# Optimization experiments

Hardware: AMD Instinct MI355X
Metric: run time of the kernel (lower is better)

## Reference

```python
import jax, jax.numpy as jnp
import numpy as np

H = 8          # num_heads
WIN = 63       # win_size
LEFT = WIN - 1 - WIN // 2  # 31
EPS = 1e-5


def layer_norm(x, w, b):
    mu = x.mean(-1, keepdims=True)
    var = ((x - mu) ** 2).mean(-1, keepdims=True)
    return (x - mu) / jnp.sqrt(var + EPS) * w + b


def setup_inputs() -> dict:
    key = jax.random.key(0)
    N, T, C = 2, 2048, 512
    hid = 4 * C
    ks = jax.random.split(key, 16)
    s = 0.02
    return {
        "x": jax.random.normal(ks[0], (N, T, C), jnp.float32),
        "norm1_w": jnp.ones((C,), jnp.float32),
        "norm1_b": jnp.zeros((C,), jnp.float32),
        "qkv_w": jax.random.normal(ks[1], (3 * C, C), jnp.float32) * s,
        "qkv_b": jnp.zeros((3 * C,), jnp.float32),
        "rel_bias": jax.random.normal(ks[2], (H, WIN), jnp.float32) * s,
        "proj_w": jax.random.normal(ks[3], (C, C), jnp.float32) * s,
        "proj_b": jnp.zeros((C,), jnp.float32),
        "norm2_w": jnp.ones((C,), jnp.float32),
        "norm2_b": jnp.zeros((C,), jnp.float32),
        "fc1_w": jax.random.normal(ks[4], (hid, C), jnp.float32) * s,
        "fc1_b": jnp.zeros((hid,), jnp.float32),
        "fc2_w": jax.random.normal(ks[5], (C, hid), jnp.float32) * s,
        "fc2_b": jnp.zeros((C,), jnp.float32),
    }


def reference(x, norm1_w, norm1_b, qkv_w, qkv_b, rel_bias, proj_w, proj_b,
              norm2_w, norm2_b, fc1_w, fc1_b, fc2_w, fc2_b):
    N, T, C = x.shape
    hd = C // H
    scale = hd ** -0.5
    right = WIN - LEFT - 1

    shortcut = x
    h = layer_norm(x, norm1_w, norm1_b)
    qkv = (h @ qkv_w.T + qkv_b).reshape(N, T, 3, H, hd)
    q, k, v = qkv[:, :, 0], qkv[:, :, 1], qkv[:, :, 2]  # (N,T,H,hd)

    # zero-pad keys/values along time, gather sliding windows
    kp = jnp.pad(k, ((0, 0), (LEFT, right), (0, 0), (0, 0)))
    vp = jnp.pad(v, ((0, 0), (LEFT, right), (0, 0), (0, 0)))
    idx = jnp.arange(T)[:, None] + jnp.arange(WIN)[None, :]
    k_win = kp[:, idx]
    v_win = vp[:, idx]

    attn = jnp.einsum('nthd,ntwhd->nhtw', q * scale, k_win)
    attn = attn + rel_bias[None, :, None, :]
    # boundary mask: key position j = t - LEFT + w must lie in [0, T)
    pos = idx - LEFT
    mask = jnp.where((pos < 0) | (pos >= T), jnp.float32(-100.0), jnp.float32(0.0))
    attn = attn + mask[None, None, :, :]
    attn = jax.nn.softmax(attn, axis=-1)

    out = jnp.einsum('nhtw,ntwhd->nthd', attn, v_win).reshape(N, T, C)
    out = out @ proj_w.T + proj_b

    x = shortcut + out
    h2 = layer_norm(x, norm2_w, norm2_b)
    m = jax.nn.gelu(h2 @ fc1_w.T + fc1_b, approximate=False)  # torch nn.GELU = exact erf
    m = m @ fc2_w.T + fc2_b
    return x + m
```

## Files before the change

kernel.cpp:

```cpp
#include <hip/hip_runtime.h>

typedef unsigned short u16;
typedef unsigned int uint;
typedef __attribute__((ext_vector_type(4))) float floatx4;
typedef __attribute__((ext_vector_type(16))) float floatx16;
typedef __attribute__((ext_vector_type(8))) short shortx8;

__device__ __forceinline__ u16 f2b(float f) {
    unsigned int u = __float_as_uint(f);
    unsigned int r = (u + 0x7fffu + ((u >> 16) & 1u)) >> 16;
    return (u16)r;
}
__device__ __forceinline__ float b2f(u16 u) {
    return __uint_as_float(((unsigned int)u) << 16);
}
__device__ __forceinline__ void gl_lds16(const u16* g, u16* l) {
    __builtin_amdgcn_global_load_lds(
        (const __attribute__((address_space(1))) void*)g,
        (__attribute__((address_space(3))) void*)l, 16, 0, 0);
}
__device__ __forceinline__ float gelu_f(float v) {
    float e = __expf(1.59576912f * v * (1.0f + 0.044715f * v * v));
    return v * e / (e + 1.0f);
}

__device__ __forceinline__ void ln_row_wave_f32(const float* __restrict__ x,
                                                const float* __restrict__ w,
                                                const float* __restrict__ b,
                                                u16* __restrict__ out, int row) {
    int lane = threadIdx.x & 63;
    const float4* xr = (const float4*)(x + (size_t)row * 512);
    float4 v0 = xr[lane * 2], v1 = xr[lane * 2 + 1];
    float s = v0.x + v0.y + v0.z + v0.w + v1.x + v1.y + v1.z + v1.w;
    float s2 = v0.x * v0.x + v0.y * v0.y + v0.z * v0.z + v0.w * v0.w +
               v1.x * v1.x + v1.y * v1.y + v1.z * v1.z + v1.w * v1.w;
    #pragma unroll
    for (int o = 32; o > 0; o >>= 1) {
        s += __shfl_xor(s, o, 64);
        s2 += __shfl_xor(s2, o, 64);
    }
    float mu = s * (1.0f / 512.0f);
    float var = s2 * (1.0f / 512.0f) - mu * mu;
    float rstd = rsqrtf(var + 1e-5f);
    const float4* wr = (const float4*)w;
    const float4* br = (const float4*)b;
    float4 w0 = wr[lane * 2], w1 = wr[lane * 2 + 1];
    float4 b0 = br[lane * 2], b1 = br[lane * 2 + 1];
    uint4 o4;
    o4.x = (uint)f2b((v0.x - mu) * rstd * w0.x + b0.x) |
           ((uint)f2b((v0.y - mu) * rstd * w0.y + b0.y) << 16);
    o4.y = (uint)f2b((v0.z - mu) * rstd * w0.z + b0.z) |
           ((uint)f2b((v0.w - mu) * rstd * w0.w + b0.w) << 16);
    o4.z = (uint)f2b((v1.x - mu) * rstd * w1.x + b1.x) |
           ((uint)f2b((v1.y - mu) * rstd * w1.y + b1.y) << 16);
    o4.w = (uint)f2b((v1.z - mu) * rstd * w1.z + b1.z) |
           ((uint)f2b((v1.w - mu) * rstd * w1.w + b1.w) << 16);
    ((uint4*)(out + (size_t)row * 512))[lane] = o4;
}

__global__ __launch_bounds__(256) void ln_kernel_b(const u16* __restrict__ x,
                                                   const float* __restrict__ w,
                                                   const float* __restrict__ b,
                                                   u16* __restrict__ out) {
    int row = blockIdx.x * 4 + (threadIdx.x >> 6);
    int lane = threadIdx.x & 63;
    uint4 p = ((const uint4*)(x + (size_t)row * 512))[lane];
    float v[8];
    v[0] = b2f((u16)(p.x & 0xffffu)); v[1] = b2f((u16)(p.x >> 16));
    v[2] = b2f((u16)(p.y & 0xffffu)); v[3] = b2f((u16)(p.y >> 16));
    v[4] = b2f((u16)(p.z & 0xffffu)); v[5] = b2f((u16)(p.z >> 16));
    v[6] = b2f((u16)(p.w & 0xffffu)); v[7] = b2f((u16)(p.w >> 16));
    float s = 0.f, s2 = 0.f;
    #pragma unroll
    for (int i = 0; i < 8; i++) { s += v[i]; s2 += v[i] * v[i]; }
    #pragma unroll
    for (int o = 32; o > 0; o >>= 1) {
        s += __shfl_xor(s, o, 64);
        s2 += __shfl_xor(s2, o, 64);
    }
    float mu = s * (1.0f / 512.0f);
    float var = s2 * (1.0f / 512.0f) - mu * mu;
    float rstd = rsqrtf(var + 1e-5f);
    const float4* wr = (const float4*)w;
    const float4* br = (const float4*)b;
    float4 w0 = wr[lane * 2], w1 = wr[lane * 2 + 1];
    float4 b0 = br[lane * 2], b1 = br[lane * 2 + 1];
    float o8[8];
    o8[0] = (v[0] - mu) * rstd * w0.x + b0.x;
    o8[1] = (v[1] - mu) * rstd * w0.y + b0.y;
    o8[2] = (v[2] - mu) * rstd * w0.z + b0.z;
    o8[3] = (v[3] - mu) * rstd * w0.w + b0.w;
    o8[4] = (v[4] - mu) * rstd * w1.x + b1.x;
    o8[5] = (v[5] - mu) * rstd * w1.y + b1.y;
    o8[6] = (v[6] - mu) * rstd * w1.z + b1.z;
    o8[7] = (v[7] - mu) * rstd * w1.w + b1.w;
    uint4 o4;
    o4.x = (uint)f2b(o8[0]) | ((uint)f2b(o8[1]) << 16);
    o4.y = (uint)f2b(o8[2]) | ((uint)f2b(o8[3]) << 16);
    o4.z = (uint)f2b(o8[4]) | ((uint)f2b(o8[5]) << 16);
    o4.w = (uint)f2b(o8[6]) | ((uint)f2b(o8[7]) << 16);
    ((uint4*)(out + (size_t)row * 512))[lane] = o4;
}

__global__ __launch_bounds__(256) void prep_kernel(
    const float* __restrict__ qkvw, u16* __restrict__ wq,
    const float* __restrict__ projw, u16* __restrict__ wp,
    const float* __restrict__ fc1w, u16* __restrict__ w1,
    const float* __restrict__ fc2w, u16* __restrict__ w2,
    const float* __restrict__ x, const float* __restrict__ n1w,
    const float* __restrict__ n1b, u16* __restrict__ hb) {
    int bi = blockIdx.x;
    if (bi < 3072) {
        const float* src;
        u16* dst;
        int i0;
        if (bi < 768)       { src = qkvw; dst = wq; i0 = bi; }
        else if (bi < 1024) { src = projw; dst = wp; i0 = bi - 768; }
        else if (bi < 2048) { src = fc1w; dst = w1; i0 = bi - 1024; }
        else                { src = fc2w; dst = w2; i0 = bi - 2048; }
        int i = i0 * 256 + threadIdx.x;
        float4 v = ((const float4*)src)[i];
        uint2 o;
        o.x = (uint)f2b(v.x) | ((uint)f2b(v.y) << 16);
        o.y = (uint)f2b(v.z) | ((uint)f2b(v.w) << 16);
        ((uint2*)dst)[i] = o;
    } else {
        int row = (bi - 3072) * 4 + (threadIdx.x >> 6);
        ln_row_wave_f32(x, n1w, n1b, hb, row);
    }
}

template <int EPI>
__global__ __launch_bounds__(256, 2) void gemm16(const u16* __restrict__ A,
                                                 const u16* __restrict__ W,
                                                 const float* __restrict__ bias,
                                                 u16* __restrict__ outB,
                                                 int M, int Nn, int K) {
    constexpr int BM = 128, BN = 128, BK = 64;
    __shared__ u16 a_s[2][BM * BK];
    __shared__ u16 b_s[2][BN * BK];

    int tid = threadIdx.x;
    int wid = tid >> 6, lane = tid & 63;
    int wm = wid >> 1, wn = wid & 1;
    int m_blk = blockIdx.x * BM;
    int n_blk = blockIdx.y * BN;
    int lr = lane & 15;
    int lkc = lane >> 4;

    floatx4 acc[4][4];
    #pragma unroll
    for (int i = 0; i < 4; i++)
        #pragma unroll
        for (int j = 0; j < 4; j++) acc[i][j] = (floatx4){0.f, 0.f, 0.f, 0.f};

    const u16* Ag = A + (size_t)m_blk * K;
    const u16* Wg = W + (size_t)n_blk * K;

    int srow = tid >> 3;
    int skc = (tid & 7) ^ (srow & 7);

    auto stage = [&](int k0, int buf) {
        #pragma unroll
        for (int p = 0; p < 4; p++)
            gl_lds16(Ag + (size_t)(p * 32 + srow) * K + k0 + skc * 8,
                     a_s[buf] + (p * 256 + tid) * 8);
        #pragma unroll
        for (int p = 0; p < 4; p++)
            gl_lds16(Wg + (size_t)(p * 32 + srow) * K + k0 + skc * 8,
                     b_s[buf] + (p * 256 + tid) * 8);
    };

    stage(0, 0);
    int nit = K >> 6;
    for (int it = 0; it < nit; it++) {
        __syncthreads();
        if (it + 1 < nit) stage((it + 1) << 6, (it + 1) & 1);
        int cb = it & 1;
        #pragma unroll
        for (int s = 0; s < 2; s++) {
            int kc = s * 4 + lkc;
            shortx8 af[4], bf[4];
            #pragma unroll
            for (int i = 0; i < 4; i++) {
                int row = wm * 64 + i * 16 + lr;
                af[i] = *(const shortx8*)(a_s[cb] + (row * 8 + (kc ^ (row & 7))) * 8);
            }
            #pragma unroll
            for (int j = 0; j < 4; j++) {
                int row = wn * 64 + j * 16 + lr;
                bf[j] = *(const shortx8*)(b_s[cb] + (row * 8 + (kc ^ (row & 7))) * 8);
            }
            #pragma unroll
            for (int i = 0; i < 4; i++)
                #pragma unroll
                for (int j = 0; j < 4; j++)
                    acc[i][j] = __builtin_amdgcn_mfma_f32_16x16x32_bf16(
                        af[i], bf[j], acc[i][j], 0, 0, 0);
        }
    }

    int col_l = lane & 15;
    int row_base = (lane >> 4) * 4;
    #pragma unroll
    for (int nj = 0; nj < 4; nj++) {
        int col = n_blk + wn * 64 + nj * 16 + col_l;
        float bv = bias[col];
        #pragma unroll
        for (int mi = 0; mi < 4; mi++) {
            #pragma unroll
            for (int r = 0; r < 4; r++) {
                int row = m_blk + wm * 64 + mi * 16 + row_base + r;
                size_t off = (size_t)row * Nn + col;
                float v = acc[mi][nj][r] + bv;
                outB[off] = f2b(EPI == 2 ? gelu_f(v) : v);
            }
        }
    }
}

template <int EPI>
__global__ __launch_bounds__(256, 2) void gemm32(const u16* __restrict__ A,
                                                 const u16* __restrict__ W,
                                                 const float* __restrict__ bias,
                                                 const float* __restrict__ residF,
                                                 const u16* __restrict__ residB,
                                                 float* __restrict__ outF,
                                                 u16* __restrict__ outB,
                                                 int M, int Nn, int K) {
    constexpr int BM = 64, BN = 64, BK = 128;
    constexpr int CPR = BK / 8, KMSK = CPR - 1;
    __shared__ u16 a_s[2][BM * BK];
    __shared__ u16 b_s[2][BN * BK];

    int tid = threadIdx.x;
    int wid = tid >> 6, lane = tid & 63;
    int wm = wid >> 1, wn = wid & 1;
    int m_blk = blockIdx.x * BM;
    int n_blk = blockIdx.y * BN;
    int lr = lane & 31;
    int lk = lane >> 5;

    floatx16 acc;
    #pragma unroll
    for (int r = 0; r < 16; r++) acc[r] = 0.f;

    const u16* Ag = A + (size_t)m_blk * K;
    const u16* Wg = W + (size_t)n_blk * K;

    int srow = tid / CPR;
    int skc = (tid & KMSK) ^ (srow & KMSK);

    auto stage = [&](int k0, int buf) {
        #pragma unroll
        for (int p = 0; p < 4; p++)
            gl_lds16(Ag + (size_t)(p * 16 + srow) * K + k0 + skc * 8,
                     a_s[buf] + (p * 256 + tid) * 8);
        #pragma unroll
        for (int p = 0; p < 4; p++)
            gl_lds16(Wg + (size_t)(p * 16 + srow) * K + k0 + skc * 8,
                     b_s[buf] + (p * 256 + tid) * 8);
    };

    stage(0, 0);
    int nit = K / BK;
    for (int it = 0; it < nit; it++) {
        __syncthreads();
        if (it + 1 < nit) stage((it + 1) * BK, (it + 1) & 1);
        int cb = it & 1;
        #pragma unroll
        for (int s = 0; s < BK / 16; s++) {
            int kc = s * 2 + lk;
            int arow = wm * 32 + lr;
            int brow = wn * 32 + lr;
            shortx8 af = *(const shortx8*)(a_s[cb] + (arow * CPR + (kc ^ (arow & KMSK))) * 8);
            shortx8 bf = *(const shortx8*)(b_s[cb] + (brow * CPR + (kc ^ (brow & KMSK))) * 8);
            acc = __builtin_amdgcn_mfma_f32_32x32x16_bf16(af, bf, acc, 0, 0, 0);
        }
    }

    int col_l = lane & 31;
    int row_q = 4 * (lane >> 5);
    int col = n_blk + wn * 32 + col_l;
    float bv = bias[col];
    #pragma unroll
    for (int r = 0; r < 16; r++) {
        int row = m_blk + wm * 32 + (r & 3) + 8 * (r >> 2) + row_q;
        size_t off = (size_t)row * Nn + col;
        float v = acc[r] + bv;
        if (EPI == 1) outB[off] = f2b(v + residF[off]);
        else          outF[off] = v + b2f(residB[off]);
    }
}

__global__ __launch_bounds__(256) void attn_kernel(const u16* __restrict__ qkv,
                                                   const float* __restrict__ rel_bias,
                                                   u16* __restrict__ out) {
    __shared__ u16 k_s[128][72];
    __shared__ u16 v_t[64][152];
    __shared__ u16 p_s[4][16][104];
    __shared__ float s_bias[64];

    int bx = blockIdx.x;
    int n = bx >> 8;
    int h = (bx >> 5) & 7;
    int t0 = (bx & 31) << 6;
    int tid = threadIdx.x, wid = tid >> 6, lane = tid & 63;
    int col = lane & 15, rq = lane >> 4;

    const u16* qrow = qkv + (size_t)(n * 2048 + t0 + wid * 16 + col) * 1536 + h * 64 + rq * 8;
    shortx8 qf0 = *(const shortx8*)qrow;
    shortx8 qf1 = *(const shortx8*)(qrow + 32);

    if (tid < 63) s_bias[tid] = rel_bias[h * 63 + tid];
    if (tid == 63) s_bias[63] = 0.f;

    const uint* qkv_u = (const uint*)qkv;
    for (int idx = tid; idx < 128 * 32; idx += 256) {
        int row = idx >> 5, j = idx & 31;
        int pos = t0 - 31 + row;
        uint kv = 0;
        if (pos >= 0 && pos < 2048)
            kv = qkv_u[(size_t)(n * 2048 + pos) * 768 + 256 + h * 32 + j];
        *(uint*)&k_s[row][j * 2] = kv;
    }
    for (int idx = tid; idx < 144 * 32; idx += 256) {
        int row = idx >> 5, j = idx & 31;
        int pos = t0 - 31 + row;
        uint vv = 0;
        if (pos >= 0 && pos < 2048)
            vv = qkv_u[(size_t)(n * 2048 + pos) * 768 + 512 + h * 32 + j];
        v_t[2 * j][row] = (u16)(vv & 0xffffu);
        v_t[2 * j + 1][row] = (u16)(vv >> 16);
    }
    __syncthreads();

    floatx4 S[5];
    #pragma unroll
    for (int nt = 0; nt < 5; nt++) S[nt] = (floatx4){0.f, 0.f, 0.f, 0.f};
    #pragma unroll
    for (int nt = 0; nt < 5; nt++) {
        const u16* kb = &k_s[wid * 16 + nt * 16 + col][rq * 8];
        shortx8 b0 = *(const shortx8*)kb;
        shortx8 b1 = *(const shortx8*)(kb + 32);
        S[nt] = __builtin_amdgcn_mfma_f32_16x16x32_bf16(qf0, b0, S[nt], 0, 0, 0);
        S[nt] = __builtin_amdgcn_mfma_f32_16x16x32_bf16(qf1, b1, S[nt], 0, 0, 0);
    }

    #pragma unroll
    for (int r = 0; r < 4; r++) {
        int t_row = rq * 4 + r;
        float sc[5];
        float mx = -1e30f;
        #pragma unroll
        for (int nt = 0; nt < 5; nt++) {
            int w = nt * 16 + col - t_row;
            int pos_abs = t0 - 31 + wid * 16 + nt * 16 + col;
            float v;
            if (w < 0 || w > 62) {
                v = -1e30f;
            } else {
                v = S[nt][r] * 0.125f + s_bias[w];
                if (pos_abs < 0 || pos_abs >= 2048) v -= 100.f;
            }
            sc[nt] = v;
            mx = fmaxf(mx, v);
        }
        #pragma unroll
        for (int o = 1; o < 16; o <<= 1) mx = fmaxf(mx, __shfl_xor(mx, o, 64));
        float l = 0.f;
        #pragma unroll
        for (int nt = 0; nt < 5; nt++) {
            sc[nt] = __expf(sc[nt] - mx);
            l += sc[nt];
        }
        #pragma unroll
        for (int o = 1; o < 16; o <<= 1) l += __shfl_xor(l, o, 64);
        float inv = 1.0f / l;
        #pragma unroll
        for (int nt = 0; nt < 5; nt++)
            p_s[wid][t_row][nt * 16 + col] = f2b(sc[nt] * inv);
        p_s[wid][t_row][80 + col] = 0;
    }
    __syncthreads();

    floatx4 O[4];
    #pragma unroll
    for (int dt = 0; dt < 4; dt++) O[dt] = (floatx4){0.f, 0.f, 0.f, 0.f};
    const u16* pr = &p_s[wid][col][rq * 8];
    shortx8 a0 = *(const shortx8*)pr;
    shortx8 a1 = *(const shortx8*)(pr + 32);
    shortx8 a2 = *(const shortx8*)(pr + 64);
    #pragma unroll
    for (int dt = 0; dt < 4; dt++) {
        const u16* vb = &v_t[dt * 16 + col][wid * 16 + rq * 8];
        shortx8 b0 = *(const shortx8*)vb;
        shortx8 b1 = *(const shortx8*)(vb + 32);
        shortx8 b2 = *(const shortx8*)(vb + 64);
        O[dt] = __builtin_amdgcn_mfma_f32_16x16x32_bf16(a0, b0, O[dt], 0, 0, 0);
        O[dt] = __builtin_amdgcn_mfma_f32_16x16x32_bf16(a1, b1, O[dt], 0, 0, 0);
        O[dt] = __builtin_amdgcn_mfma_f32_16x16x32_bf16(a2, b2, O[dt], 0, 0, 0);
    }

    #pragma unroll
    for (int dt = 0; dt < 4; dt++) {
        #pragma unroll
        for (int r = 0; r < 4; r++) {
            int t_row = rq * 4 + r;
            out[(size_t)(n * 2048 + t0 + wid * 16 + t_row) * 512 + h * 64 + dt * 16 + col] =
                f2b(O[dt][r]);
        }
    }
}

extern "C" void kernel_launch(void* const* d_in, const int* in_sizes, int n_in,
                              void* d_out, int out_size, void* d_ws, size_t ws_size,
                              hipStream_t stream) {
    const float* x     = (const float*)d_in[0];
    const float* n1w   = (const float*)d_in[1];
    const float* n1b   = (const float*)d_in[2];
    const float* qkvw  = (const float*)d_in[3];
    const float* qkvbv = (const float*)d_in[4];
    const float* relb  = (const float*)d_in[5];
    const float* projw = (const float*)d_in[6];
    const float* projb = (const float*)d_in[7];
    const float* n2w   = (const float*)d_in[8];
    const float* n2b   = (const float*)d_in[9];
    const float* fc1w  = (const float*)d_in[10];
    const float* fc1b  = (const float*)d_in[11];
    const float* fc2w  = (const float*)d_in[12];
    const float* fc2b  = (const float*)d_in[13];
    float* out = (float*)d_out;

    char* p = (char*)d_ws;
    u16* wq   = (u16*)p;  p += (size_t)786432 * 2;
    u16* wp   = (u16*)p;  p += (size_t)262144 * 2;
    u16* w1   = (u16*)p;  p += (size_t)1048576 * 2;
    u16* w2   = (u16*)p;  p += (size_t)1048576 * 2;
    u16* hb   = (u16*)p;  p += (size_t)2097152 * 2;
    u16* qkvb = (u16*)p;  p += (size_t)6291456 * 2;
    u16* attb = (u16*)p;  p += (size_t)2097152 * 2;
    u16* x2b  = (u16*)p;  p += (size_t)2097152 * 2;
    u16* mb   = (u16*)p;  p += (size_t)8388608 * 2;

    prep_kernel<<<4096, 256, 0, stream>>>(qkvw, wq, projw, wp, fc1w, w1, fc2w, w2,
                                          x, n1w, n1b, hb);
    gemm16<0><<<dim3(32, 12), 256, 0, stream>>>(hb, wq, qkvbv, qkvb, 4096, 1536, 512);
    attn_kernel<<<512, 256, 0, stream>>>(qkvb, relb, attb);
    gemm32<1><<<dim3(64, 8), 256, 0, stream>>>(attb, wp, projb, x, nullptr,
                                               nullptr, x2b, 4096, 512, 512);
    ln_kernel_b<<<1024, 256, 0, stream>>>(x2b, n2w, n2b, hb);
    gemm16<2><<<dim3(32, 16), 256, 0, stream>>>(hb, w1, fc1b, mb, 4096, 2048, 512);
    gemm32<3><<<dim3(64, 8), 256, 0, stream>>>(mb, w2, fc2b, nullptr, x2b,
                                               out, nullptr, 4096, 512, 2048);
}
```

Baseline: 167.6 us.

## Drop double buffering in GEMMs and switch small GEMM to 16x16 MFMA tiles

Both GEMM kernels drop their double-buffered LDS staging and become single-buffered, with a sync before and after each K-tile compute. The 64x64 GEMM also moves from one 32x32x16 MFMA per wave with BK=128 to four 16x16x32 MFMAs per wave with BK=64. Launch bounds rise to 3 and 4 blocks per CU. The aim is to cut LDS use and raise occupancy so that other resident blocks hide memory latency, in place of in-block prefetch. The cost is that loads and compute no longer overlap within a block, and each tile needs twice as many barriers.

```diff
diff --git a/kernel.cpp b/kernel.cpp
--- a/kernel.cpp
+++ b/kernel.cpp
@@ -3,7 +3,6 @@
 typedef unsigned short u16;
 typedef unsigned int uint;
 typedef __attribute__((ext_vector_type(4))) float floatx4;
-typedef __attribute__((ext_vector_type(16))) float floatx16;
 typedef __attribute__((ext_vector_type(8))) short shortx8;
 
 __device__ __forceinline__ u16 f2b(float f) {
@@ -131,20 +130,19 @@
 }
 
 template <int EPI>
-__global__ __launch_bounds__(256, 2) void gemm16(const u16* __restrict__ A,
+__global__ __launch_bounds__(256, 3) void gemm16(const u16* __restrict__ A,
                                                  const u16* __restrict__ W,
                                                  const float* __restrict__ bias,
                                                  u16* __restrict__ outB,
                                                  int M, int Nn, int K) {
-    constexpr int BM = 128, BN = 128, BK = 64;
-    __shared__ u16 a_s[2][BM * BK];
-    __shared__ u16 b_s[2][BN * BK];
+    __shared__ u16 a_s[128 * 64];
+    __shared__ u16 b_s[128 * 64];
 
     int tid = threadIdx.x;
     int wid = tid >> 6, lane = tid & 63;
     int wm = wid >> 1, wn = wid & 1;
-    int m_blk = blockIdx.x * BM;
-    int n_blk = blockIdx.y * BN;
+    int m_blk = blockIdx.x * 128;
+    int n_blk = blockIdx.y * 128;
     int lr = lane & 15;
     int lkc = lane >> 4;
 
@@ -160,23 +158,16 @@
     int srow = tid >> 3;
     int skc = (tid & 7) ^ (srow & 7);
 
-    auto stage = [&](int k0, int buf) {
+    for (int k0 = 0; k0 < K; k0 += 64) {
         #pragma unroll
         for (int p = 0; p < 4; p++)
             gl_lds16(Ag + (size_t)(p * 32 + srow) * K + k0 + skc * 8,
-                     a_s[buf] + (p * 256 + tid) * 8);
+                     a_s + (p * 256 + tid) * 8);
         #pragma unroll
         for (int p = 0; p < 4; p++)
             gl_lds16(Wg + (size_t)(p * 32 + srow) * K + k0 + skc * 8,
-                     b_s[buf] + (p * 256 + tid) * 8);
-    };
-
-    stage(0, 0);
-    int nit = K >> 6;
-    for (int it = 0; it < nit; it++) {
+                     b_s + (p * 256 + tid) * 8);
         __syncthreads();
-        if (it + 1 < nit) stage((it + 1) << 6, (it + 1) & 1);
-        int cb = it & 1;
         #pragma unroll
         for (int s = 0; s < 2; s++) {
             int kc = s * 4 + lkc;
@@ -184,12 +175,12 @@
             #pragma unroll
             for (int i = 0; i < 4; i++) {
                 int row = wm * 64 + i * 16 + lr;
-                af[i] = *(const shortx8*)(a_s[cb] + (row * 8 + (kc ^ (row & 7))) * 8);
+                af[i] = *(const shortx8*)(a_s + (row * 8 + (kc ^ (row & 7))) * 8);
             }
             #pragma unroll
             for (int j = 0; j < 4; j++) {
                 int row = wn * 64 + j * 16 + lr;
-                bf[j] = *(const shortx8*)(b_s[cb] + (row * 8 + (kc ^ (row & 7))) * 8);
+                bf[j] = *(const shortx8*)(b_s + (row * 8 + (kc ^ (row & 7))) * 8);
             }
             #pragma unroll
             for (int i = 0; i < 4; i++)
@@ -198,6 +189,7 @@
                     acc[i][j] = __builtin_amdgcn_mfma_f32_16x16x32_bf16(
                         af[i], bf[j], acc[i][j], 0, 0, 0);
         }
+        __syncthreads();
     }
 
     int col_l = lane & 15;
@@ -220,7 +212,7 @@
 }
 
 template <int EPI>
-__global__ __launch_bounds__(256, 2) void gemm32(const u16* __restrict__ A,
+__global__ __launch_bounds__(256, 4) void gemm64(const u16* __restrict__ A,
                                                  const u16* __restrict__ W,
                                                  const float* __restrict__ bias,
                                                  const float* __restrict__ residF,
@@ -228,68 +220,80 @@
                                                  float* __restrict__ outF,
                                                  u16* __restrict__ outB,
                                                  int M, int Nn, int K) {
-    constexpr int BM = 64, BN = 64, BK = 128;
-    constexpr int CPR = BK / 8, KMSK = CPR - 1;
-    __shared__ u16 a_s[2][BM * BK];
-    __shared__ u16 b_s[2][BN * BK];
+    __shared__ u16 a_s[64 * 64];
+    __shared__ u16 b_s[64 * 64];
 
     int tid = threadIdx.x;
     int wid = tid >> 6, lane = tid & 63;
     int wm = wid >> 1, wn = wid & 1;
-    int m_blk = blockIdx.x * BM;
-    int n_blk = blockIdx.y * BN;
-    int lr = lane & 31;
-    int lk = lane >> 5;
-
-    floatx16 acc;
-    #pragma unroll
-    for (int r = 0; r < 16; r++) acc[r] = 0.f;
+    int m_blk = blockIdx.x * 64;
+    int n_blk = blockIdx.y * 64;
+    int lr = lane & 15;
+    int lkc = lane >> 4;
+
+    floatx4 acc[2][2];
+    #pragma unroll
+    for (int i = 0; i < 2; i++)
+        #pragma unroll
+        for (int j = 0; j < 2; j++) acc[i][j] = (floatx4){0.f, 0.f, 0.f, 0.f};
 
     const u16* Ag = A + (size_t)m_blk * K;
     const u16* Wg = W + (size_t)n_blk * K;
 
-    int srow = tid / CPR;
-    int skc = (tid & KMSK) ^ (srow & KMSK);
-
-    auto stage = [&](int k0, int buf) {
-        #pragma unroll
-        for (int p = 0; p < 4; p++)
-            gl_lds16(Ag + (size_t)(p * 16 + srow) * K + k0 + skc * 8,
-                     a_s[buf] + (p * 256 + tid) * 8);
-        #pragma unroll
-        for (int p = 0; p < 4; p++)
-            gl_lds16(Wg + (size_t)(p * 16 + srow) * K + k0 + skc * 8,
-                     b_s[buf] + (p * 256 + tid) * 8);
-    };
-
-    stage(0, 0);
-    int nit = K / BK;
-    for (int it = 0; it < nit; it++) {
+    int srow = tid >> 3;
+    int skc = (tid & 7) ^ (srow & 7);
+
+    for (int k0 = 0; k0 < K; k0 += 64) {
+        #pragma unroll
+        for (int p = 0; p < 2; p++)
+            gl_lds16(Ag + (size_t)(p * 32 + srow) * K + k0 + skc * 8,
+                     a_s + (p * 256 + tid) * 8);
+        #pragma unroll
+        for (int p = 0; p < 2; p++)
+            gl_lds16(Wg + (size_t)(p * 32 + srow) * K + k0 + skc * 8,
+                     b_s + (p * 256 + tid) * 8);
         __syncthreads();
-        if (it + 1 < nit) stage((it + 1) * BK, (it + 1) & 1);
-        int cb = it & 1;
-        #pragma unroll
-        for (int s = 0; s < BK / 16; s++) {
-            int kc = s * 2 + lk;
-            int arow = wm * 32 + lr;
-            int brow = wn * 32 + lr;
-            shortx8 af = *(const shortx8*)(a_s[cb] + (arow * CPR + (kc ^ (arow & KMSK))) * 8);
-            shortx8 bf = *(const shortx8*)(b_s[cb] + (brow * CPR + (kc ^ (brow & KMSK))) * 8);
-            acc = __builtin_amdgcn_mfma_f32_32x32x16_bf16(af, bf, acc, 0, 0, 0);
-        }
-    }
-
-    int col_l = lane & 31;
-    int row_q = 4 * (lane >> 5);
-    int col = n_blk + wn * 32 + col_l;
-    float bv = bias[col];
-    #pragma unroll
-    for (int r = 0; r < 16; r++) {
-        int row = m_blk + wm * 32 + (r & 3) + 8 * (r >> 2) + row_q;
-        size_t off = (size_t)row * Nn + col;
-        float v = acc[r] + bv;
-        if (EPI == 1) outB[off] = f2b(v + residF[off]);
-        else          outF[off] = v + b2f(residB[off]);
+        #pragma unroll
+        for (int s = 0; s < 2; s++) {
+            int kc = s * 4 + lkc;
+            shortx8 af[2], bf[2];
+            #pragma unroll
+            for (int i = 0; i < 2; i++) {
+                int row = wm * 32 + i * 16 + lr;
+                af[i] = *(const shortx8*)(a_s + (row * 8 + (kc ^ (row & 7))) * 8);
+            }
+            #pragma unroll
+            for (int j = 0; j < 2; j++) {
+                int row = wn * 32 + j * 16 + lr;
+                bf[j] = *(const shortx8*)(b_s + (row * 8 + (kc ^ (row & 7))) * 8);
+            }
+            #pragma unroll
+            for (int i = 0; i < 2; i++)
+                #pragma unroll
+                for (int j = 0; j < 2; j++)
+                    acc[i][j] = __builtin_amdgcn_mfma_f32_16x16x32_bf16(
+                        af[i], bf[j], acc[i][j], 0, 0, 0);
+        }
+        __syncthreads();
+    }
+
+    int col_l = lane & 15;
+    int row_base = (lane >> 4) * 4;
+    #pragma unroll
+    for (int nj = 0; nj < 2; nj++) {
+        int col = n_blk + wn * 32 + nj * 16 + col_l;
+        float bv = bias[col];
+        #pragma unroll
+        for (int mi = 0; mi < 2; mi++) {
+            #pragma unroll
+            for (int r = 0; r < 4; r++) {
+                int row = m_blk + wm * 32 + mi * 16 + row_base + r;
+                size_t off = (size_t)row * Nn + col;
+                float v = acc[mi][nj][r] + bv;
+                if (EPI == 1) outB[off] = f2b(v + residF[off]);
+                else          outF[off] = v + b2f(residB[off]);
+            }
+        }
     }
 }
 
@@ -447,10 +451,10 @@
                                           x, n1w, n1b, hb);
     gemm16<0><<<dim3(32, 12), 256, 0, stream>>>(hb, wq, qkvbv, qkvb, 4096, 1536, 512);
     attn_kernel<<<512, 256, 0, stream>>>(qkvb, relb, attb);
-    gemm32<1><<<dim3(64, 8), 256, 0, stream>>>(attb, wp, projb, x, nullptr,
+    gemm64<1><<<dim3(64, 8), 256, 0, stream>>>(attb, wp, projb, x, nullptr,
                                                nullptr, x2b, 4096, 512, 512);
     ln_kernel_b<<<1024, 256, 0, stream>>>(x2b, n2w, n2b, hb);
     gemm16<2><<<dim3(32, 16), 256, 0, stream>>>(hb, w1, fc1b, mb, 4096, 2048, 512);
-    gemm32<3><<<dim3(64, 8), 256, 0, stream>>>(mb, w2, fc2b, nullptr, x2b,
+    gemm64<3><<<dim3(64, 8), 256, 0, stream>>>(mb, w2, fc2b, nullptr, x2b,
                                                out, nullptr, 4096, 512, 2048);
 }
```

Measured after the change: 173.2 us. 1.03x slower.
